# Performance work log

Measured on AMD Instinct MI355X. Metric: run time of the kernel, lower is better.

Reference implementation:

```python
import jax, jax.numpy as jnp
import numpy as np

N_NODES = 50000
EPS = 1e-12  # F.normalize eps


def sage_conv(x, src, dst, W_l, b_l, W_r):
    # PyG SAGEConv: out = lin_l(mean_j x_j) + lin_r(x_i), then L2 normalize.
    n = x.shape[0]
    agg = jax.ops.segment_sum(x[src], dst, num_segments=n)          # [N, d]
    cnt = jax.ops.segment_sum(jnp.ones_like(src, dtype=x.dtype), dst,
                              num_segments=n)                       # [N]
    mean = agg / jnp.maximum(cnt, 1.0)[:, None]
    out = mean @ W_l.T + b_l + x @ W_r.T
    norm = jnp.linalg.norm(out, axis=-1, keepdims=True)
    return out / jnp.maximum(norm, EPS)


def setup_inputs() -> dict:
    key = jax.random.key(0)
    ks = jax.random.split(key, 8)
    nfeat, nhid, nclass = 64, 64, 10
    E = 1250000
    features = jax.random.normal(ks[0], (N_NODES, nfeat), dtype=jnp.float32)
    edge_index = jax.random.randint(ks[1], (2, E), 0, N_NODES, dtype=jnp.int64)
    s1 = 1.0 / np.sqrt(nfeat)
    s2 = 1.0 / np.sqrt(nhid)
    return {
        "features": features,
        "edge_index": edge_index,
        "W1_l": jax.random.normal(ks[2], (nhid, nfeat), dtype=jnp.float32) * s1,
        "b1": jnp.zeros((nhid,), dtype=jnp.float32),
        "W1_r": jax.random.normal(ks[3], (nhid, nfeat), dtype=jnp.float32) * s1,
        "W2_l": jax.random.normal(ks[4], (nclass, nhid), dtype=jnp.float32) * s2,
        "b2": jnp.zeros((nclass,), dtype=jnp.float32),
        "W2_r": jax.random.normal(ks[5], (nclass, nhid), dtype=jnp.float32) * s2,
    }


def reference(features, edge_index, W1_l, b1, W1_r, W2_l, b2, W2_r):
    src, dst = edge_index[0], edge_index[1]
    x = jax.nn.relu(sage_conv(features, src, dst, W1_l, b1, W1_r))
    # dropout is identity in eval mode
    x = sage_conv(x, src, dst, W2_l, b2, W2_r)
    return jax.nn.log_softmax(x, axis=1)
```

## Files before the change

kernel.cpp:

```cpp
#include <hip/hip_runtime.h>
#include <hip/hip_bf16.h>


static constexpr int FEAT = 64;
static constexpr int SLOTS = 64;
static constexpr int BUCK_SZ = 6250;

__device__ __forceinline__ float4 f4add(float4 a, float4 b) {
  return make_float4(a.x + b.x, a.y + b.y, a.z + b.z, a.w + b.w);
}
__device__ __forceinline__ unsigned short f2bf(float f) {
  __hip_bfloat16 h = __float2bfloat16(f);
  return *reinterpret_cast<unsigned short*>(&h);
}
__device__ __forceinline__ float bfl(unsigned int u) {
  return __uint_as_float(u << 16);
}
__device__ __forceinline__ float bfh(unsigned int u) {
  return __uint_as_float(u & 0xFFFF0000u);
}

__global__ __launch_bounds__(256) void dense1_fill_kernel(
    const float* __restrict__ x,
    const float* __restrict__ Wl, const float* __restrict__ Wr,
    const float* __restrict__ b,
    unsigned short* __restrict__ p, float* __restrict__ q, int N,
    const int* __restrict__ src, const int* __restrict__ dst,
    int* __restrict__ cursor, int* __restrict__ col, int E,
    int dense_blocks, int nbx) {
  __shared__ float4 Ws[16 * 16];
  int tid = threadIdx.x;

  if ((int)blockIdx.x >= dense_blocks) {
    int fb = (int)blockIdx.x - dense_blocks;
    int bk = fb & 7;
    int e = (fb >> 3) * 256 + tid;
    if (e < E) {
      int d = __builtin_nontemporal_load(dst + e);
      int lo = bk * BUCK_SZ;
      if (d >= lo && d < lo + BUCK_SZ) {
        int s = __builtin_nontemporal_load(src + e);
        int pos = atomicAdd(&cursor[d], 1);
        if (pos < SLOTS) col[d * SLOTS + pos] = s;
      }
    }
    return;
  }

  int bx = (int)blockIdx.x % nbx;
  int by = (int)blockIdx.x / nbx;
  int mat = by >> 2;
  int og = by & 3;
  const float4* Wg = (const float4*)(mat ? Wr : Wl);
  Ws[tid] = Wg[(og * 16) * 16 + tid];
  __syncthreads();

  int node = bx * 256 + tid;
  if (node >= N) return;

  const float4* X4 = (const float4*)x + (size_t)node * 16;
  float4 xr[16];
#pragma unroll
  for (int kq = 0; kq < 16; ++kq) xr[kq] = X4[kq];

  float acc[16];
#pragma unroll 4
  for (int o = 0; o < 16; ++o) {
    float a = 0.0f;
#pragma unroll
    for (int kq = 0; kq < 16; ++kq) {
      float4 w = Ws[o * 16 + kq];
      float4 xv = xr[kq];
      a = fmaf(xv.x, w.x, fmaf(xv.y, w.y, fmaf(xv.z, w.z, fmaf(xv.w, w.w, a))));
    }
    acc[o] = a;
  }

  if (mat) {
    float4* O4 = (float4*)(q + (size_t)node * FEAT + og * 16);
    const float4* B4 = (const float4*)(b + og * 16);
#pragma unroll
    for (int oq = 0; oq < 4; ++oq) {
      float4 bv = B4[oq];
      O4[oq] = make_float4(acc[oq * 4] + bv.x, acc[oq * 4 + 1] + bv.y,
                           acc[oq * 4 + 2] + bv.z, acc[oq * 4 + 3] + bv.w);
    }
  } else {
    uint4 w0, w1;
    w0.x = f2bf(acc[0]) | ((unsigned)f2bf(acc[1]) << 16);
    w0.y = f2bf(acc[2]) | ((unsigned)f2bf(acc[3]) << 16);
    w0.z = f2bf(acc[4]) | ((unsigned)f2bf(acc[5]) << 16);
    w0.w = f2bf(acc[6]) | ((unsigned)f2bf(acc[7]) << 16);
    w1.x = f2bf(acc[8]) | ((unsigned)f2bf(acc[9]) << 16);
    w1.y = f2bf(acc[10]) | ((unsigned)f2bf(acc[11]) << 16);
    w1.z = f2bf(acc[12]) | ((unsigned)f2bf(acc[13]) << 16);
    w1.w = f2bf(acc[14]) | ((unsigned)f2bf(acc[15]) << 16);
    uint4* O = (uint4*)p + (size_t)node * 8 + og * 2;
    O[0] = w0;
    O[1] = w1;
  }
}

__global__ __launch_bounds__(256) void gather1_kernel(
    const int* __restrict__ cursor, const int* __restrict__ col,
    const uint4* __restrict__ p1, float* __restrict__ qh, int N) {
  int tid = threadIdx.x;
  int wave = tid >> 6, lane = tid & 63;
  int g = lane >> 3, q = lane & 7;
  int node = blockIdx.x * 4 + wave;
  if (node >= N) return;

  int deg = cursor[node];
  int cnt = min(deg, SLOTS);
  int beg = node * SLOTS;
  int end = beg + cnt;

  float a[8];
#pragma unroll
  for (int j = 0; j < 8; ++j) a[j] = 0.0f;

  int e = beg + g;
  for (; e + 8 < end; e += 16) {
    int s0 = col[e], s1 = col[e + 8];
    uint4 w0 = p1[(size_t)s0 * 8 + q];
    uint4 w1 = p1[(size_t)s1 * 8 + q];
    a[0] += bfl(w0.x); a[1] += bfh(w0.x); a[2] += bfl(w0.y); a[3] += bfh(w0.y);
    a[4] += bfl(w0.z); a[5] += bfh(w0.z); a[6] += bfl(w0.w); a[7] += bfh(w0.w);
    a[0] += bfl(w1.x); a[1] += bfh(w1.x); a[2] += bfl(w1.y); a[3] += bfh(w1.y);
    a[4] += bfl(w1.z); a[5] += bfh(w1.z); a[6] += bfl(w1.w); a[7] += bfh(w1.w);
  }
  if (e < end) {
    uint4 w0 = p1[(size_t)col[e] * 8 + q];
    a[0] += bfl(w0.x); a[1] += bfh(w0.x); a[2] += bfl(w0.y); a[3] += bfh(w0.y);
    a[4] += bfl(w0.z); a[5] += bfh(w0.z); a[6] += bfl(w0.w); a[7] += bfh(w0.w);
  }

#pragma unroll
  for (int off = 8; off <= 32; off <<= 1) {
#pragma unroll
    for (int j = 0; j < 8; ++j) a[j] += __shfl_xor(a[j], off);
  }

  float invc = 1.0f / (float)max(deg, 1);
  const float4* Q4 = (const float4*)qh + (size_t)node * 16 + q * 2;
  float4 q0 = Q4[0], q1 = Q4[1];
  float v[8];
  v[0] = fmaf(a[0], invc, q0.x); v[1] = fmaf(a[1], invc, q0.y);
  v[2] = fmaf(a[2], invc, q0.z); v[3] = fmaf(a[3], invc, q0.w);
  v[4] = fmaf(a[4], invc, q1.x); v[5] = fmaf(a[5], invc, q1.y);
  v[6] = fmaf(a[6], invc, q1.z); v[7] = fmaf(a[7], invc, q1.w);

  float ss = 0.0f;
#pragma unroll
  for (int j = 0; j < 8; ++j) ss += v[j] * v[j];
#pragma unroll
  for (int off = 1; off <= 4; off <<= 1) ss += __shfl_xor(ss, off);
  float scale = 1.0f / fmaxf(sqrtf(ss), 1e-12f);

  if (g == 0) {
    float4* O4 = (float4*)qh + (size_t)node * 16 + q * 2;
    O4[0] = make_float4(fmaxf(v[0] * scale, 0.f), fmaxf(v[1] * scale, 0.f),
                        fmaxf(v[2] * scale, 0.f), fmaxf(v[3] * scale, 0.f));
    O4[1] = make_float4(fmaxf(v[4] * scale, 0.f), fmaxf(v[5] * scale, 0.f),
                        fmaxf(v[6] * scale, 0.f), fmaxf(v[7] * scale, 0.f));
  }
}

__global__ __launch_bounds__(256) void dense2_kernel(
    const float* __restrict__ h,
    const float* __restrict__ Wl, const float* __restrict__ Wr,
    const float* __restrict__ b,
    float* __restrict__ p2, float* __restrict__ q2, int N) {
  __shared__ float4 Wls[10 * 16];
  __shared__ float4 Wrs[10 * 16];
  __shared__ float bs[10];
  int tid = threadIdx.x;
  if (tid < 160) {
    Wls[tid] = ((const float4*)Wl)[tid];
    Wrs[tid] = ((const float4*)Wr)[tid];
  }
  if (tid < 10) bs[tid] = b[tid];
  __syncthreads();

  int node = blockIdx.x * 256 + tid;
  if (node >= N) return;

  const float4* H4 = (const float4*)h + (size_t)node * 16;
  float4 hr[16];
#pragma unroll
  for (int kq = 0; kq < 16; ++kq) hr[kq] = H4[kq];

  float pa[10], qa[10];
#pragma unroll 1
  for (int c = 0; c < 10; ++c) {
    float ap = 0.0f, aq = 0.0f;
#pragma unroll
    for (int kq = 0; kq < 16; ++kq) {
      float4 wl = Wls[c * 16 + kq];
      float4 wr = Wrs[c * 16 + kq];
      float4 hv = hr[kq];
      ap = fmaf(hv.x, wl.x, fmaf(hv.y, wl.y, fmaf(hv.z, wl.z, fmaf(hv.w, wl.w, ap))));
      aq = fmaf(hv.x, wr.x, fmaf(hv.y, wr.y, fmaf(hv.z, wr.z, fmaf(hv.w, wr.w, aq))));
    }
    pa[c] = ap;
    qa[c] = aq;
  }

  float4* P4 = (float4*)(p2 + (size_t)node * 16);
  float4* Q4 = (float4*)(q2 + (size_t)node * 16);
  P4[0] = make_float4(pa[0], pa[1], pa[2], pa[3]);
  P4[1] = make_float4(pa[4], pa[5], pa[6], pa[7]);
  P4[2] = make_float4(pa[8], pa[9], 0.f, 0.f);
  P4[3] = make_float4(0.f, 0.f, 0.f, 0.f);
  Q4[0] = make_float4(qa[0] + bs[0], qa[1] + bs[1], qa[2] + bs[2], qa[3] + bs[3]);
  Q4[1] = make_float4(qa[4] + bs[4], qa[5] + bs[5], qa[6] + bs[6], qa[7] + bs[7]);
  Q4[2] = make_float4(qa[8] + bs[8], qa[9] + bs[9], 0.f, 0.f);
  Q4[3] = make_float4(0.f, 0.f, 0.f, 0.f);
}

__global__ __launch_bounds__(256) void gather2_kernel(
    const int* __restrict__ cursor, const int* __restrict__ col,
    const float* __restrict__ p2, const float* __restrict__ q2,
    float* __restrict__ out, int N) {
  int tid = threadIdx.x;
  int wave = tid >> 6, lane = tid & 63;
  int g = lane >> 2, q = lane & 3;
  int node = blockIdx.x * 4 + wave;
  if (node >= N) return;

  int deg = cursor[node];
  int cnt = min(deg, SLOTS);
  int beg = node * SLOTS;
  int end = beg + cnt;
  const float4* P4 = (const float4*)p2;

  float4 acc = make_float4(0.f, 0.f, 0.f, 0.f);
  int e = beg + g;
  for (; e + 16 < end; e += 32) {
    int s0 = col[e], s1 = col[e + 16];
    float4 v0 = P4[(size_t)s0 * 4 + q];
    float4 v1 = P4[(size_t)s1 * 4 + q];
    acc = f4add(acc, f4add(v0, v1));
  }
  if (e < end) {
    int s = col[e];
    acc = f4add(acc, P4[(size_t)s * 4 + q]);
  }

#pragma unroll
  for (int off = 4; off <= 32; off <<= 1) {
    acc.x += __shfl_xor(acc.x, off);
    acc.y += __shfl_xor(acc.y, off);
    acc.z += __shfl_xor(acc.z, off);
    acc.w += __shfl_xor(acc.w, off);
  }

  float invc = 1.0f / (float)max(deg, 1);
  float4 qv = ((const float4*)q2)[(size_t)node * 4 + q];
  float4 v = make_float4(fmaf(acc.x, invc, qv.x), fmaf(acc.y, invc, qv.y),
                         fmaf(acc.z, invc, qv.z), fmaf(acc.w, invc, qv.w));

  float ss = v.x * v.x + v.y * v.y + v.z * v.z + v.w * v.w;
  ss += __shfl_xor(ss, 1);
  ss += __shfl_xor(ss, 2);
  float scale = 1.0f / fmaxf(sqrtf(ss), 1e-12f);
  v.x *= scale; v.y *= scale; v.z *= scale; v.w *= scale;

  float m;
  if (q < 2)       m = fmaxf(fmaxf(v.x, v.y), fmaxf(v.z, v.w));
  else if (q == 2) m = fmaxf(v.x, v.y);
  else             m = -1e30f;
  m = fmaxf(m, __shfl_xor(m, 1));
  m = fmaxf(m, __shfl_xor(m, 2));

  float es;
  if (q < 2)       es = __expf(v.x - m) + __expf(v.y - m) + __expf(v.z - m) + __expf(v.w - m);
  else if (q == 2) es = __expf(v.x - m) + __expf(v.y - m);
  else             es = 0.0f;
  es += __shfl_xor(es, 1);
  es += __shfl_xor(es, 2);
  float lse = m + __logf(es);

  if (g == 0 && q < 3) {
    float2* o = (float2*)(out + (size_t)node * 10);
    if (q < 2) {
      o[q * 2]     = make_float2(v.x - lse, v.y - lse);
      o[q * 2 + 1] = make_float2(v.z - lse, v.w - lse);
    } else {
      o[4] = make_float2(v.x - lse, v.y - lse);
    }
  }
}

extern "C" void kernel_launch(void* const* d_in, const int* in_sizes, int n_in,
                              void* d_out, int out_size, void* d_ws, size_t ws_size,
                              hipStream_t stream) {
  const float* features = (const float*)d_in[0];
  const int* edge_index = (const int*)d_in[1];
  const float* W1_l = (const float*)d_in[2];
  const float* b1   = (const float*)d_in[3];
  const float* W1_r = (const float*)d_in[4];
  const float* W2_l = (const float*)d_in[5];
  const float* b2   = (const float*)d_in[6];
  const float* W2_r = (const float*)d_in[7];
  float* out = (float*)d_out;

  const int N = in_sizes[0] / FEAT;
  const int E = in_sizes[1] / 2;
  const int* src = edge_index;
  const int* dst = edge_index + E;

  char* ws = (char*)d_ws;
  int* cursor            = (int*)(ws + 0);
  int* col               = (int*)(ws + 200064);
  unsigned short* p1     = (unsigned short*)(ws + 13000064);
  float* q1h1            = (float*)(ws + 19400064);
  float* p2              = (float*)(ws + 32200064);
  float* q2              = (float*)(ws + 35400064);

  hipMemsetAsync(cursor, 0, (size_t)N * sizeof(int), stream);

  int eb8 = ((E + 255) / 256) * 8;
  int nb256 = (N + 255) / 256;
  int nbw = (N + 3) / 4;
  int dense_blocks = nb256 * 8;

  dense1_fill_kernel<<<dense_blocks + eb8, 256, 0, stream>>>(
      features, W1_l, W1_r, b1, p1, q1h1, N,
      src, dst, cursor, col, E, dense_blocks, nb256);
  gather1_kernel<<<nbw, 256, 0, stream>>>(cursor, col, (const uint4*)p1, q1h1, N);
  dense2_kernel<<<nb256, 256, 0, stream>>>(q1h1, W2_l, W2_r, b2, p2, q2, N);
  gather2_kernel<<<nbw, 256, 0, stream>>>(cursor, col, p2, q2, out, N);
}
```

Baseline: 232.7 us.

## Fuse layer-2 dense into gather1, store p2 as bf16, persistent fill blocks

Merges the layer-1 gather/normalize/ReLU with the layer-2 dense projection so the hidden activations never round-trip through global memory, and drops one kernel launch. The layer-2 neighbour projection p2 is stored in bf16 at 32 bytes per node instead of 64 bytes of fp32, which halves gather2's random-read traffic. Fill blocks are now a fixed persistent grid placed before the dense blocks and loop over edge chunks. The costs are lower precision in the second aggregation and extra shuffle reductions across the 10 output columns in the fused kernel.

Result: slower. 270.7 us (+16.4%).

```diff
diff --git a/kernel.cpp b/kernel.cpp
--- a/kernel.cpp
+++ b/kernel.cpp
@@ -5,6 +5,7 @@
 static constexpr int FEAT = 64;
 static constexpr int SLOTS = 64;
 static constexpr int BUCK_SZ = 6250;
+static constexpr int FILL_PB = 400;
 
 __device__ __forceinline__ float4 f4add(float4 a, float4 b) {
   return make_float4(a.x + b.x, a.y + b.y, a.z + b.z, a.w + b.w);
@@ -12,6 +13,9 @@
 __device__ __forceinline__ unsigned short f2bf(float f) {
   __hip_bfloat16 h = __float2bfloat16(f);
   return *reinterpret_cast<unsigned short*>(&h);
+}
+__device__ __forceinline__ unsigned int pk2(float a, float b) {
+  return (unsigned)f2bf(a) | ((unsigned)f2bf(b) << 16);
 }
 __device__ __forceinline__ float bfl(unsigned int u) {
   return __uint_as_float(u << 16);
@@ -27,28 +31,32 @@
     unsigned short* __restrict__ p, float* __restrict__ q, int N,
     const int* __restrict__ src, const int* __restrict__ dst,
     int* __restrict__ cursor, int* __restrict__ col, int E,
-    int dense_blocks, int nbx) {
+    int fill_blocks, int nbx, int nchunks) {
   __shared__ float4 Ws[16 * 16];
   int tid = threadIdx.x;
 
-  if ((int)blockIdx.x >= dense_blocks) {
-    int fb = (int)blockIdx.x - dense_blocks;
+  if ((int)blockIdx.x < fill_blocks) {
+    int fb = (int)blockIdx.x;
     int bk = fb & 7;
-    int e = (fb >> 3) * 256 + tid;
-    if (e < E) {
-      int d = __builtin_nontemporal_load(dst + e);
-      int lo = bk * BUCK_SZ;
-      if (d >= lo && d < lo + BUCK_SZ) {
-        int s = __builtin_nontemporal_load(src + e);
-        int pos = atomicAdd(&cursor[d], 1);
-        if (pos < SLOTS) col[d * SLOTS + pos] = s;
+    int blk = fb >> 3;
+    int lo = bk * BUCK_SZ;
+    for (int chunk = blk; chunk < nchunks; chunk += FILL_PB) {
+      int e = chunk * 256 + tid;
+      if (e < E) {
+        int d = __builtin_nontemporal_load(dst + e);
+        if (d >= lo && d < lo + BUCK_SZ) {
+          int s = __builtin_nontemporal_load(src + e);
+          int pos = atomicAdd(&cursor[d], 1);
+          if (pos < SLOTS) col[d * SLOTS + pos] = s;
+        }
       }
     }
     return;
   }
 
-  int bx = (int)blockIdx.x % nbx;
-  int by = (int)blockIdx.x / nbx;
+  int db = (int)blockIdx.x - fill_blocks;
+  int bx = db % nbx;
+  int by = db / nbx;
   int mat = by >> 2;
   int og = by & 3;
   const float4* Wg = (const float4*)(mat ? Wr : Wl);
@@ -87,24 +95,37 @@
     }
   } else {
     uint4 w0, w1;
-    w0.x = f2bf(acc[0]) | ((unsigned)f2bf(acc[1]) << 16);
-    w0.y = f2bf(acc[2]) | ((unsigned)f2bf(acc[3]) << 16);
-    w0.z = f2bf(acc[4]) | ((unsigned)f2bf(acc[5]) << 16);
-    w0.w = f2bf(acc[6]) | ((unsigned)f2bf(acc[7]) << 16);
-    w1.x = f2bf(acc[8]) | ((unsigned)f2bf(acc[9]) << 16);
-    w1.y = f2bf(acc[10]) | ((unsigned)f2bf(acc[11]) << 16);
-    w1.z = f2bf(acc[12]) | ((unsigned)f2bf(acc[13]) << 16);
-    w1.w = f2bf(acc[14]) | ((unsigned)f2bf(acc[15]) << 16);
+    w0.x = pk2(acc[0], acc[1]);
+    w0.y = pk2(acc[2], acc[3]);
+    w0.z = pk2(acc[4], acc[5]);
+    w0.w = pk2(acc[6], acc[7]);
+    w1.x = pk2(acc[8], acc[9]);
+    w1.y = pk2(acc[10], acc[11]);
+    w1.z = pk2(acc[12], acc[13]);
+    w1.w = pk2(acc[14], acc[15]);
     uint4* O = (uint4*)p + (size_t)node * 8 + og * 2;
     O[0] = w0;
     O[1] = w1;
   }
 }
 
-__global__ __launch_bounds__(256) void gather1_kernel(
+__global__ __launch_bounds__(256) void gather1_dense2_kernel(
     const int* __restrict__ cursor, const int* __restrict__ col,
-    const uint4* __restrict__ p1, float* __restrict__ qh, int N) {
+    const uint4* __restrict__ p1, const float* __restrict__ qh,
+    const float* __restrict__ W2l, const float* __restrict__ W2r,
+    const float* __restrict__ b2,
+    uint4* __restrict__ p2, float* __restrict__ q2, int N) {
+  __shared__ float4 Wls[10 * 16];
+  __shared__ float4 Wrs[10 * 16];
+  __shared__ float bs[10];
   int tid = threadIdx.x;
+  if (tid < 160) {
+    Wls[tid] = ((const float4*)W2l)[tid];
+    Wrs[tid] = ((const float4*)W2r)[tid];
+  }
+  if (tid < 10) bs[tid] = b2[tid];
+  __syncthreads();
+
   int wave = tid >> 6, lane = tid & 63;
   int g = lane >> 3, q = lane & 7;
   int node = blockIdx.x * 4 + wave;
@@ -157,74 +178,64 @@
   for (int off = 1; off <= 4; off <<= 1) ss += __shfl_xor(ss, off);
   float scale = 1.0f / fmaxf(sqrtf(ss), 1e-12f);
 
-  if (g == 0) {
-    float4* O4 = (float4*)qh + (size_t)node * 16 + q * 2;
-    O4[0] = make_float4(fmaxf(v[0] * scale, 0.f), fmaxf(v[1] * scale, 0.f),
-                        fmaxf(v[2] * scale, 0.f), fmaxf(v[3] * scale, 0.f));
-    O4[1] = make_float4(fmaxf(v[4] * scale, 0.f), fmaxf(v[5] * scale, 0.f),
-                        fmaxf(v[6] * scale, 0.f), fmaxf(v[7] * scale, 0.f));
-  }
-}
-
-__global__ __launch_bounds__(256) void dense2_kernel(
-    const float* __restrict__ h,
-    const float* __restrict__ Wl, const float* __restrict__ Wr,
-    const float* __restrict__ b,
-    float* __restrict__ p2, float* __restrict__ q2, int N) {
-  __shared__ float4 Wls[10 * 16];
-  __shared__ float4 Wrs[10 * 16];
-  __shared__ float bs[10];
-  int tid = threadIdx.x;
-  if (tid < 160) {
-    Wls[tid] = ((const float4*)Wl)[tid];
-    Wrs[tid] = ((const float4*)Wr)[tid];
-  }
-  if (tid < 10) bs[tid] = b[tid];
-  __syncthreads();
-
-  int node = blockIdx.x * 256 + tid;
-  if (node >= N) return;
-
-  const float4* H4 = (const float4*)h + (size_t)node * 16;
-  float4 hr[16];
-#pragma unroll
-  for (int kq = 0; kq < 16; ++kq) hr[kq] = H4[kq];
+  float hv[8];
+#pragma unroll
+  for (int j = 0; j < 8; ++j) hv[j] = fmaxf(v[j] * scale, 0.0f);
 
   float pa[10], qa[10];
-#pragma unroll 1
+#pragma unroll 2
   for (int c = 0; c < 10; ++c) {
+    float4 l0 = Wls[c * 16 + q * 2], l1 = Wls[c * 16 + q * 2 + 1];
+    float4 r0 = Wrs[c * 16 + q * 2], r1 = Wrs[c * 16 + q * 2 + 1];
     float ap = 0.0f, aq = 0.0f;
-#pragma unroll
-    for (int kq = 0; kq < 16; ++kq) {
-      float4 wl = Wls[c * 16 + kq];
-      float4 wr = Wrs[c * 16 + kq];
-      float4 hv = hr[kq];
-      ap = fmaf(hv.x, wl.x, fmaf(hv.y, wl.y, fmaf(hv.z, wl.z, fmaf(hv.w, wl.w, ap))));
-      aq = fmaf(hv.x, wr.x, fmaf(hv.y, wr.y, fmaf(hv.z, wr.z, fmaf(hv.w, wr.w, aq))));
-    }
+    ap = fmaf(hv[0], l0.x, fmaf(hv[1], l0.y, fmaf(hv[2], l0.z, fmaf(hv[3], l0.w, ap))));
+    ap = fmaf(hv[4], l1.x, fmaf(hv[5], l1.y, fmaf(hv[6], l1.z, fmaf(hv[7], l1.w, ap))));
+    aq = fmaf(hv[0], r0.x, fmaf(hv[1], r0.y, fmaf(hv[2], r0.z, fmaf(hv[3], r0.w, aq))));
+    aq = fmaf(hv[4], r1.x, fmaf(hv[5], r1.y, fmaf(hv[6], r1.z, fmaf(hv[7], r1.w, aq))));
     pa[c] = ap;
     qa[c] = aq;
   }
-
-  float4* P4 = (float4*)(p2 + (size_t)node * 16);
-  float4* Q4 = (float4*)(q2 + (size_t)node * 16);
-  P4[0] = make_float4(pa[0], pa[1], pa[2], pa[3]);
-  P4[1] = make_float4(pa[4], pa[5], pa[6], pa[7]);
-  P4[2] = make_float4(pa[8], pa[9], 0.f, 0.f);
-  P4[3] = make_float4(0.f, 0.f, 0.f, 0.f);
-  Q4[0] = make_float4(qa[0] + bs[0], qa[1] + bs[1], qa[2] + bs[2], qa[3] + bs[3]);
-  Q4[1] = make_float4(qa[4] + bs[4], qa[5] + bs[5], qa[6] + bs[6], qa[7] + bs[7]);
-  Q4[2] = make_float4(qa[8] + bs[8], qa[9] + bs[9], 0.f, 0.f);
-  Q4[3] = make_float4(0.f, 0.f, 0.f, 0.f);
+#pragma unroll
+  for (int off = 1; off <= 4; off <<= 1) {
+#pragma unroll
+    for (int c = 0; c < 10; ++c) {
+      pa[c] += __shfl_xor(pa[c], off);
+      qa[c] += __shfl_xor(qa[c], off);
+    }
+  }
+
+  if (g == 0) {
+    if (q == 0) {
+      uint4 w;
+      w.x = pk2(pa[0], pa[1]); w.y = pk2(pa[2], pa[3]);
+      w.z = pk2(pa[4], pa[5]); w.w = pk2(pa[6], pa[7]);
+      p2[(size_t)node * 2] = w;
+    } else if (q == 1) {
+      uint4 w;
+      w.x = pk2(pa[8], pa[9]); w.y = 0u; w.z = 0u; w.w = 0u;
+      p2[(size_t)node * 2 + 1] = w;
+    } else if (q == 2) {
+      ((float4*)q2)[(size_t)node * 4] =
+          make_float4(qa[0] + bs[0], qa[1] + bs[1], qa[2] + bs[2], qa[3] + bs[3]);
+    } else if (q == 3) {
+      ((float4*)q2)[(size_t)node * 4 + 1] =
+          make_float4(qa[4] + bs[4], qa[5] + bs[5], qa[6] + bs[6], qa[7] + bs[7]);
+    } else if (q == 4) {
+      ((float4*)q2)[(size_t)node * 4 + 2] =
+          make_float4(qa[8] + bs[8], qa[9] + bs[9], 0.f, 0.f);
+    } else if (q == 5) {
+      ((float4*)q2)[(size_t)node * 4 + 3] = make_float4(0.f, 0.f, 0.f, 0.f);
+    }
+  }
 }
 
 __global__ __launch_bounds__(256) void gather2_kernel(
     const int* __restrict__ cursor, const int* __restrict__ col,
-    const float* __restrict__ p2, const float* __restrict__ q2,
+    const uint4* __restrict__ p2, const float* __restrict__ q2,
     float* __restrict__ out, int N) {
   int tid = threadIdx.x;
   int wave = tid >> 6, lane = tid & 63;
-  int g = lane >> 2, q = lane & 3;
+  int g = lane >> 1, q = lane & 1;
   int node = blockIdx.x * 4 + wave;
   if (node >= N) return;
 
@@ -232,62 +243,79 @@
   int cnt = min(deg, SLOTS);
   int beg = node * SLOTS;
   int end = beg + cnt;
-  const float4* P4 = (const float4*)p2;
-
-  float4 acc = make_float4(0.f, 0.f, 0.f, 0.f);
+
+  float a[8];
+#pragma unroll
+  for (int j = 0; j < 8; ++j) a[j] = 0.0f;
+
   int e = beg + g;
-  for (; e + 16 < end; e += 32) {
-    int s0 = col[e], s1 = col[e + 16];
-    float4 v0 = P4[(size_t)s0 * 4 + q];
-    float4 v1 = P4[(size_t)s1 * 4 + q];
-    acc = f4add(acc, f4add(v0, v1));
+  for (; e + 32 < end; e += 64) {
+    int s0 = col[e], s1 = col[e + 32];
+    uint4 w0 = p2[(size_t)s0 * 2 + q];
+    uint4 w1 = p2[(size_t)s1 * 2 + q];
+    a[0] += bfl(w0.x); a[1] += bfh(w0.x); a[2] += bfl(w0.y); a[3] += bfh(w0.y);
+    a[4] += bfl(w0.z); a[5] += bfh(w0.z); a[6] += bfl(w0.w); a[7] += bfh(w0.w);
+    a[0] += bfl(w1.x); a[1] += bfh(w1.x); a[2] += bfl(w1.y); a[3] += bfh(w1.y);
+    a[4] += bfl(w1.z); a[5] += bfh(w1.z); a[6] += bfl(w1.w); a[7] += bfh(w1.w);
   }
   if (e < end) {
-    int s = col[e];
-    acc = f4add(acc, P4[(size_t)s * 4 + q]);
-  }
-
-#pragma unroll
-  for (int off = 4; off <= 32; off <<= 1) {
-    acc.x += __shfl_xor(acc.x, off);
-    acc.y += __shfl_xor(acc.y, off);
-    acc.z += __shfl_xor(acc.z, off);
-    acc.w += __shfl_xor(acc.w, off);
+    uint4 w0 = p2[(size_t)col[e] * 2 + q];
+    a[0] += bfl(w0.x); a[1] += bfh(w0.x); a[2] += bfl(w0.y); a[3] += bfh(w0.y);
+    a[4] += bfl(w0.z); a[5] += bfh(w0.z); a[6] += bfl(w0.w); a[7] += bfh(w0.w);
+  }
+
+#pragma unroll
+  for (int off = 2; off <= 32; off <<= 1) {
+#pragma unroll
+    for (int j = 0; j < 8; ++j) a[j] += __shfl_xor(a[j], off);
   }
 
   float invc = 1.0f / (float)max(deg, 1);
-  float4 qv = ((const float4*)q2)[(size_t)node * 4 + q];
-  float4 v = make_float4(fmaf(acc.x, invc, qv.x), fmaf(acc.y, invc, qv.y),
-                         fmaf(acc.z, invc, qv.z), fmaf(acc.w, invc, qv.w));
-
-  float ss = v.x * v.x + v.y * v.y + v.z * v.z + v.w * v.w;
+  const float4* Q4 = (const float4*)q2 + (size_t)node * 4 + q * 2;
+  float4 q0 = Q4[0], q1 = Q4[1];
+  float v[8];
+  v[0] = fmaf(a[0], invc, q0.x); v[1] = fmaf(a[1], invc, q0.y);
+  v[2] = fmaf(a[2], invc, q0.z); v[3] = fmaf(a[3], invc, q0.w);
+  v[4] = fmaf(a[4], invc, q1.x); v[5] = fmaf(a[5], invc, q1.y);
+  v[6] = fmaf(a[6], invc, q1.z); v[7] = fmaf(a[7], invc, q1.w);
+
+  float ss = 0.0f;
+#pragma unroll
+  for (int j = 0; j < 8; ++j) ss += v[j] * v[j];
   ss += __shfl_xor(ss, 1);
-  ss += __shfl_xor(ss, 2);
   float scale = 1.0f / fmaxf(sqrtf(ss), 1e-12f);
-  v.x *= scale; v.y *= scale; v.z *= scale; v.w *= scale;
+#pragma unroll
+  for (int j = 0; j < 8; ++j) v[j] *= scale;
 
   float m;
-  if (q < 2)       m = fmaxf(fmaxf(v.x, v.y), fmaxf(v.z, v.w));
-  else if (q == 2) m = fmaxf(v.x, v.y);
-  else             m = -1e30f;
+  if (q == 0) {
+    m = v[0];
+#pragma unroll
+    for (int j = 1; j < 8; ++j) m = fmaxf(m, v[j]);
+  } else {
+    m = fmaxf(v[0], v[1]);
+  }
   m = fmaxf(m, __shfl_xor(m, 1));
-  m = fmaxf(m, __shfl_xor(m, 2));
-
-  float es;
-  if (q < 2)       es = __expf(v.x - m) + __expf(v.y - m) + __expf(v.z - m) + __expf(v.w - m);
-  else if (q == 2) es = __expf(v.x - m) + __expf(v.y - m);
-  else             es = 0.0f;
+
+  float es = 0.0f;
+  if (q == 0) {
+#pragma unroll
+    for (int j = 0; j < 8; ++j) es += __expf(v[j] - m);
+  } else {
+    es = __expf(v[0] - m) + __expf(v[1] - m);
+  }
   es += __shfl_xor(es, 1);
-  es += __shfl_xor(es, 2);
   float lse = m + __logf(es);
 
-  if (g == 0 && q < 3) {
+  if (g == 0) {
     float2* o = (float2*)(out + (size_t)node * 10);
-    if (q < 2) {
-      o[q * 2]     = make_float2(v.x - lse, v.y - lse);
-      o[q * 2 + 1] = make_float2(v.z - lse, v.w - lse);
+    if (q == 0) {
+      o[0] = make_float2(v[0] - lse, v[1] - lse);
+      o[1] = make_float2(v[2] - lse, v[3] - lse);
+      o[2] = make_float2(v[4] - lse, v[5] - lse);
+      o[3] = make_float2(v[6] - lse, v[7] - lse);
     } else {
-      o[4] = make_float2(v.x - lse, v.y - lse);
+      o[4] = make_float2(v[0] - lse, v[1] - lse);
     }
   }
 }
@@ -314,21 +342,22 @@
   int* cursor            = (int*)(ws + 0);
   int* col               = (int*)(ws + 200064);
   unsigned short* p1     = (unsigned short*)(ws + 13000064);
-  float* q1h1            = (float*)(ws + 19400064);
-  float* p2              = (float*)(ws + 32200064);
-  float* q2              = (float*)(ws + 35400064);
+  float* q1              = (float*)(ws + 19400064);
+  uint4* p2              = (uint4*)(ws + 32200064);
+  float* q2              = (float*)(ws + 33800064);
 
   hipMemsetAsync(cursor, 0, (size_t)N * sizeof(int), stream);
 
-  int eb8 = ((E + 255) / 256) * 8;
+  int nchunks = (E + 255) / 256;
+  int fill_blocks = 8 * FILL_PB;
   int nb256 = (N + 255) / 256;
   int nbw = (N + 3) / 4;
   int dense_blocks = nb256 * 8;
 
-  dense1_fill_kernel<<<dense_blocks + eb8, 256, 0, stream>>>(
-      features, W1_l, W1_r, b1, p1, q1h1, N,
-      src, dst, cursor, col, E, dense_blocks, nb256);
-  gather1_kernel<<<nbw, 256, 0, stream>>>(cursor, col, (const uint4*)p1, q1h1, N);
-  dense2_kernel<<<nb256, 256, 0, stream>>>(q1h1, W2_l, W2_r, b2, p2, q2, N);
-  gather2_kernel<<<nbw, 256, 0, stream>>>(cursor, col, p2, q2, out, N);
-}
+  dense1_fill_kernel<<<fill_blocks + dense_blocks, 256, 0, stream>>>(
+      features, W1_l, W1_r, b1, p1, q1, N,
+      src, dst, cursor, col, E, fill_blocks, nb256, nchunks);
+  gather1_dense2_kernel<<<nbw, 256, 0, stream>>>(
+      cursor, col, (const uint4*)p1, q1, W2_l, W2_r, b2, p2, q2, N);
+  gather2_kernel<<<nbw, 256, 0, stream>>>(cursor, col, (const uint4*)p2, q2, out, N);
+}
```
